# Optimization experiments

Hardware: AMD Instinct MI355X
Metric: run time of the kernel (lower is better)

## Reference

```python
import jax, jax.numpy as jnp
import numpy as np

N = 50000   # nodes
E = 800000  # edges
B = 64      # graphs in batch
IN = 128    # in_features
HID = 64    # hidden_channels
H = 4       # head_count
C = 10      # out_classes
NEG = 0.2   # leaky relu negative slope
EPS = 1e-5  # batchnorm eps (eval mode, running mean 0 / var 1)


def _gat(x, edge_index, W, a_src, a_dst, b):
    """PyG GATConv (add_self_loops=False, concat=True), eval mode (no dropout)."""
    Hh, F = a_src.shape
    xW = (x @ W).reshape(-1, Hh, F)                       # [N,H,F]
    src, dst = edge_index[0], edge_index[1]
    e = (jnp.einsum('nhf,hf->nh', xW, a_src)[src]
         + jnp.einsum('nhf,hf->nh', xW, a_dst)[dst])      # [E,H]
    e = jnp.where(e > 0, e, NEG * e)                      # leaky relu
    m = jax.ops.segment_max(e, dst, num_segments=N)       # per-dst max
    m = jnp.where(jnp.isfinite(m), m, 0.0)
    p = jnp.exp(e - m[dst])
    denom = jax.ops.segment_sum(p, dst, num_segments=N)
    alpha = p / jnp.maximum(denom[dst], 1e-16)            # edge softmax over dst
    out = jax.ops.segment_sum(alpha[:, :, None] * xW[src], dst, num_segments=N)
    return out.reshape(-1, Hh * F) + b


def _bn_relu(y, g, be):
    # BatchNorm1d in eval mode with running_mean=0, running_var=1, then ReLU
    return jax.nn.relu(g * y / jnp.sqrt(1.0 + EPS) + be)


def setup_inputs():
    key = jax.random.key(0)
    ks = jax.random.split(key, 24)
    s = lambda k, shape: (jax.random.normal(k, shape, jnp.float32) * 0.05)
    z = lambda shape: jnp.zeros(shape, jnp.float32)
    o = lambda shape: jnp.ones(shape, jnp.float32)
    return {
        'acc_flag': 0,
        'x': jax.random.normal(ks[0], (N, IN), jnp.float32),
        'edge_index': jax.random.randint(ks[1], (2, E), 0, N),
        'batch': jnp.sort(jax.random.randint(ks[2], (N,), 0, B)),
        # layer 1: GATConv(IN -> HID, heads=H, concat)
        'W1': s(ks[3], (IN, H * HID)), 'a_src1': s(ks[4], (H, HID)), 'a_dst1': s(ks[5], (H, HID)), 'b1': z((H * HID,)),
        # proj: GATConv(H*HID -> HID, heads=1) + BN
        'W2': s(ks[6], (H * HID, HID)), 'a_src2': s(ks[7], (1, HID)), 'a_dst2': s(ks[8], (1, HID)), 'b2': z((HID,)), 'g2': o((HID,)), 'be2': z((HID,)),
        # block 1
        'W3': s(ks[9], (HID, HID)), 'a_src3': s(ks[10], (1, HID)), 'a_dst3': s(ks[11], (1, HID)), 'b3': z((HID,)), 'g3': o((HID,)), 'be3': z((HID,)),
        # block 2
        'W4': s(ks[12], (HID, HID)), 'a_src4': s(ks[13], (1, HID)), 'a_dst4': s(ks[14], (1, HID)), 'b4': z((HID,)), 'g4': o((HID,)), 'be4': z((HID,)),
        # MLP head
        'Wh1': s(ks[15], (HID, 128)), 'bh1': z((128,)),
        'Wh2': s(ks[16], (128, C)), 'bh2': z((C,)),
    }


def reference(acc_flag, x, edge_index, batch,
              W1, a_src1, a_dst1, b1,
              W2, a_src2, a_dst2, b2, g2, be2,
              W3, a_src3, a_dst3, b3, g3, be3,
              W4, a_src4, a_dst4, b4, g4, be4,
              Wh1, bh1, Wh2, bh2):
    # hardware GAT layer + ReLU (relu applied twice in original -> idempotent)
    x1 = jax.nn.relu(_gat(x, edge_index, W1, a_src1, a_dst1, b1))   # [N, H*HID]
    # projection block: residual base is zeros (shape mismatch H*HID vs HID)
    h = _bn_relu(_gat(x1, edge_index, W2, a_src2, a_dst2, b2), g2, be2)
    # residual blocks (shapes match -> x + relu(bn(y)))
    h = h + _bn_relu(_gat(h, edge_index, W3, a_src3, a_dst3, b3), g3, be3)
    h = h + _bn_relu(_gat(h, edge_index, W4, a_src4, a_dst4, b4), g4, be4)
    # global mean pool over graphs
    pooled = jax.ops.segment_sum(h, batch, num_segments=B)
    cnt = jnp.maximum(jax.ops.segment_sum(jnp.ones((N,), h.dtype), batch, num_segments=B), 1.0)
    hp = pooled / cnt[:, None]                                      # [B, HID]
    # MLP head
    return jax.nn.relu(hp @ Wh1 + bh1) @ Wh2 + bh2                  # [B, C]
```

## Files before the change

### kernel.cpp

```cpp
#include <hip/hip_runtime.h>

#define N_NODES 50000
#define N_EDGES 800000
#define N_GRAPHS 64
#define F_IN 128
#define F_HID 64
#define N_HEADS 4
#define N_CLASSES 10
#define NEG_SLOPE 0.2f
#define BN_RSQ 0.9999950000374997f

typedef __bf16 bf16x8 __attribute__((ext_vector_type(8)));
typedef float floatx4 __attribute__((ext_vector_type(4)));

__device__ __forceinline__ float lrelu(float v) { return v > 0.0f ? v : NEG_SLOPE * v; }

__device__ __forceinline__ float b2f(unsigned short u) {
    return __uint_as_float(((unsigned int)u) << 16);
}
__device__ __forceinline__ unsigned short f2b(float f) {
    unsigned int u = __float_as_uint(f);
    return (unsigned short)((u + 0x7fffu + ((u >> 16) & 1u)) >> 16);
}
__device__ __forceinline__ float blo(unsigned int d) { return __uint_as_float(d << 16); }
__device__ __forceinline__ float bhi(unsigned int d) { return __uint_as_float(d & 0xffff0000u); }

__global__ void k_deg(const int* __restrict__ ei, int* __restrict__ deg) {
    int e = blockIdx.x * blockDim.x + threadIdx.x;
    if (e < N_EDGES) atomicAdd(&deg[ei[N_EDGES + e]], 1);
}

__global__ void k_offs(const int* __restrict__ deg, int* __restrict__ offs,
                       int* __restrict__ total) {
    int i = blockIdx.x * blockDim.x + threadIdx.x;
    int lane = threadIdx.x & 63;
    int v = (i < N_NODES) ? deg[i] : 0;
    int incl = v;
    for (int o = 1; o < 64; o <<= 1) {
        int t = __shfl_up(incl, o);
        if (lane >= o) incl += t;
    }
    int wtot = __shfl(incl, 63);
    int base = 0;
    if (lane == 0) base = atomicAdd(total, wtot);
    base = __shfl(base, 0);
    if (i < N_NODES) offs[i] = base + incl - v;
}

__global__ void k_fill(const int* __restrict__ ei, const int* __restrict__ offs,
                       int* __restrict__ cur, int* __restrict__ csr_src) {
    int e = blockIdx.x * blockDim.x + threadIdx.x;
    if (e < N_EDGES) {
        int d = ei[N_EDGES + e];
        int pos = offs[d] + atomicAdd(&cur[d], 1);
        csr_src[pos] = ei[e];
    }
}

__global__ void k_bounds(const int* __restrict__ batch, int* __restrict__ bounds) {
    int g = threadIdx.x;
    if (g > N_GRAPHS) return;
    int lo = 0, hi = N_NODES;
    while (lo < hi) {
        int mid = (lo + hi) >> 1;
        if (batch[mid] < g) lo = mid + 1; else hi = mid;
    }
    bounds[g] = lo;
}

__global__ void k_prepw(const float* __restrict__ W, unsigned short* __restrict__ Wt,
                        int K, int N) {
    int i = blockIdx.x * blockDim.x + threadIdx.x;
    if (i < K * N) {
        int k = i / N, n = i % N;
        Wt[n * K + k] = f2b(W[i]);
    }
}

template <int K, int N, int HEADS, bool AF32>
__global__ __launch_bounds__(256) void k_mgemm(const void* __restrict__ Ap,
                                               const unsigned short* __restrict__ Bt,
                                               const float* __restrict__ asrc,
                                               const float* __restrict__ adst,
                                               unsigned short* __restrict__ out,
                                               float* __restrict__ es,
                                               float* __restrict__ ed, int rows) {
    constexpr int LDP = K + 8;
    __shared__ unsigned short As[64 * LDP];
    const int tid = threadIdx.x;
    const int r0 = blockIdx.x * 64;
    if (AF32) {
        const float* A = (const float*)Ap;
        for (int i = tid; i < 16 * K; i += 256) {
            int r = i / (K / 4), c4 = i % (K / 4);
            int row = r0 + r;
            float4 v = (row < rows) ? *(const float4*)&A[(size_t)row * K + c4 * 4]
                                    : make_float4(0.f, 0.f, 0.f, 0.f);
            ushort4 u;
            u.x = f2b(v.x); u.y = f2b(v.y); u.z = f2b(v.z); u.w = f2b(v.w);
            *(ushort4*)&As[r * LDP + c4 * 4] = u;
        }
    } else {
        const unsigned short* A = (const unsigned short*)Ap;
        for (int i = tid; i < 8 * K; i += 256) {
            int r = i / (K / 8), c8 = i % (K / 8);
            int row = r0 + r;
            uint4 v;
            if (row < rows) v = *(const uint4*)&A[(size_t)row * K + c8 * 8];
            else { v.x = v.y = v.z = v.w = 0; }
            *(uint4*)&As[r * LDP + c8 * 8] = v;
        }
    }
    __syncthreads();
    const int w = tid >> 6, lane = tid & 63;
    const int quad = lane >> 4, l16 = lane & 15;
    const int gr0 = r0 + w * 16 + quad * 4;
    bf16x8 afrag[K / 32];
#pragma unroll
    for (int kk = 0; kk < K / 32; ++kk)
        afrag[kk] = *(const bf16x8*)&As[(w * 16 + l16) * LDP + kk * 32 + quad * 8];
    float sacc[4] = {0.f, 0.f, 0.f, 0.f};
    float dacc[4] = {0.f, 0.f, 0.f, 0.f};
#pragma unroll 1
    for (int ct = 0; ct < N / 16; ++ct) {
        floatx4 acc = {0.f, 0.f, 0.f, 0.f};
#pragma unroll
        for (int kk = 0; kk < K / 32; ++kk) {
            const bf16x8 bfrag =
                *(const bf16x8*)&Bt[(size_t)(ct * 16 + l16) * K + kk * 32 + quad * 8];
            acc = __builtin_amdgcn_mfma_f32_16x16x32_bf16(afrag[kk], bfrag, acc, 0, 0, 0);
        }
        const int gc = ct * 16 + l16;
        const int hh = gc >> 6;
        const float av = asrc[gc & (64 * HEADS > N ? N - 1 : 63) + (hh << 6) - (hh << 6)
                              ];
        (void)av;
        {
            const int f = gc & 63;
            const float as = asrc[hh * 64 + f];
            const float ad = adst[hh * 64 + f];
#pragma unroll
            for (int rg = 0; rg < 4; ++rg) {
                sacc[rg] = fmaf(acc[rg], as, sacc[rg]);
                dacc[rg] = fmaf(acc[rg], ad, dacc[rg]);
            }
        }
#pragma unroll
        for (int rg = 0; rg < 4; ++rg) {
            int gr = gr0 + rg;
            if (gr < rows) out[(size_t)gr * N + gc] = f2b(acc[rg]);
        }
        if ((ct & 3) == 3) {
#pragma unroll
            for (int rg = 0; rg < 4; ++rg) {
                float s = sacc[rg], d = dacc[rg];
                for (int o = 1; o < 16; o <<= 1) {
                    s += __shfl_xor(s, o);
                    d += __shfl_xor(d, o);
                }
                if (l16 == 0) {
                    int gr = gr0 + rg;
                    if (gr < rows) {
                        es[(size_t)gr * HEADS + hh] = s;
                        ed[(size_t)gr * HEADS + hh] = d;
                    }
                }
                sacc[rg] = 0.f;
                dacc[rg] = 0.f;
            }
        }
    }
}

__global__ __launch_bounds__(256) void k_gat1(
    const unsigned short* __restrict__ xW, const float* __restrict__ es, const float* __restrict__ ed,
    const int* __restrict__ offs, const int* __restrict__ deg, const int* __restrict__ csr,
    const float* __restrict__ bias, unsigned short* __restrict__ out) {
    __shared__ float ps[4][256];
    __shared__ int sbuf[4][64];
    const int wv = threadIdx.x >> 6;
    const int lane = threadIdx.x & 63;
    const int n = blockIdx.x * 4 + wv;
    if (n >= N_NODES) return;
    const int off = offs[n];
    const int dg = deg[n];
    const float4 edv = *(const float4*)&ed[n * 4];
    const int t = lane & 15, grp = lane >> 4, hq = t >> 2;

    float acc[16];
#pragma unroll
    for (int k = 0; k < 16; ++k) acc[k] = 0.f;
    float d0 = 0.f, d1 = 0.f, d2 = 0.f, d3 = 0.f;

    for (int base = 0; base < dg; base += 64) {
        const int idx = base + lane;
        int s_l = 0;
        float p0 = 0.f, p1 = 0.f, p2 = 0.f, p3 = 0.f;
        if (idx < dg) {
            s_l = csr[off + idx];
            const float4 ev = *(const float4*)&es[s_l * 4];
            p0 = __expf(lrelu(ev.x + edv.x));
            p1 = __expf(lrelu(ev.y + edv.y));
            p2 = __expf(lrelu(ev.z + edv.z));
            p3 = __expf(lrelu(ev.w + edv.w));
        }
        d0 += p0; d1 += p1; d2 += p2; d3 += p3;
        *(float4*)&ps[wv][lane * 4] = make_float4(p0, p1, p2, p3);
        sbuf[wv][lane] = s_l;
        const int cnt = min(64, dg - base);
        const int cntR = (cnt + 7) & ~7;
        for (int j4 = 0; j4 < cntR; j4 += 8) {
            const int ja = j4 + grp;
            const int jb = ja + 4;
            const float pa = ps[wv][ja * 4 + hq];
            const float pb = ps[wv][jb * 4 + hq];
            const int sa = sbuf[wv][ja];
            const int sb = sbuf[wv][jb];
            const uint4 a0 = *(const uint4*)&xW[(size_t)sa * 256 + t * 16];
            const uint4 a1 = *(const uint4*)&xW[(size_t)sa * 256 + t * 16 + 8];
            const uint4 b0 = *(const uint4*)&xW[(size_t)sb * 256 + t * 16];
            const uint4 b1 = *(const uint4*)&xW[(size_t)sb * 256 + t * 16 + 8];
            acc[0]  = fmaf(pa, blo(a0.x), acc[0]);
            acc[1]  = fmaf(pa, bhi(a0.x), acc[1]);
            acc[2]  = fmaf(pa, blo(a0.y), acc[2]);
            acc[3]  = fmaf(pa, bhi(a0.y), acc[3]);
            acc[4]  = fmaf(pa, blo(a0.z), acc[4]);
            acc[5]  = fmaf(pa, bhi(a0.z), acc[5]);
            acc[6]  = fmaf(pa, blo(a0.w), acc[6]);
            acc[7]  = fmaf(pa, bhi(a0.w), acc[7]);
            acc[8]  = fmaf(pa, blo(a1.x), acc[8]);
            acc[9]  = fmaf(pa, bhi(a1.x), acc[9]);
            acc[10] = fmaf(pa, blo(a1.y), acc[10]);
            acc[11] = fmaf(pa, bhi(a1.y), acc[11]);
            acc[12] = fmaf(pa, blo(a1.z), acc[12]);
            acc[13] = fmaf(pa, bhi(a1.z), acc[13]);
            acc[14] = fmaf(pa, blo(a1.w), acc[14]);
            acc[15] = fmaf(pa, bhi(a1.w), acc[15]);
            acc[0]  = fmaf(pb, blo(b0.x), acc[0]);
            acc[1]  = fmaf(pb, bhi(b0.x), acc[1]);
            acc[2]  = fmaf(pb, blo(b0.y), acc[2]);
            acc[3]  = fmaf(pb, bhi(b0.y), acc[3]);
            acc[4]  = fmaf(pb, blo(b0.z), acc[4]);
            acc[5]  = fmaf(pb, bhi(b0.z), acc[5]);
            acc[6]  = fmaf(pb, blo(b0.w), acc[6]);
            acc[7]  = fmaf(pb, bhi(b0.w), acc[7]);
            acc[8]  = fmaf(pb, blo(b1.x), acc[8]);
            acc[9]  = fmaf(pb, bhi(b1.x), acc[9]);
            acc[10] = fmaf(pb, blo(b1.y), acc[10]);
            acc[11] = fmaf(pb, bhi(b1.y), acc[11]);
            acc[12] = fmaf(pb, blo(b1.z), acc[12]);
            acc[13] = fmaf(pb, bhi(b1.z), acc[13]);
            acc[14] = fmaf(pb, blo(b1.w), acc[14]);
            acc[15] = fmaf(pb, bhi(b1.w), acc[15]);
        }
    }
#pragma unroll
    for (int k = 0; k < 16; ++k) {
        acc[k] += __shfl_xor(acc[k], 16);
        acc[k] += __shfl_xor(acc[k], 32);
    }
    for (int o = 1; o < 64; o <<= 1) {
        d0 += __shfl_xor(d0, o);
        d1 += __shfl_xor(d1, o);
        d2 += __shfl_xor(d2, o);
        d3 += __shfl_xor(d3, o);
    }
    if (grp == 0) {
        const float dsel = hq == 0 ? d0 : hq == 1 ? d1 : hq == 2 ? d2 : d3;
        const float inv = 1.0f / fmaxf(dsel, 1e-16f);
#pragma unroll
        for (int k4 = 0; k4 < 16; k4 += 4) {
            const int c = t * 16 + k4;
            const float4 bv = *(const float4*)&bias[c];
            ushort4 o4;
            o4.x = f2b(fmaxf(fmaf(acc[k4 + 0], inv, bv.x), 0.f));
            o4.y = f2b(fmaxf(fmaf(acc[k4 + 1], inv, bv.y), 0.f));
            o4.z = f2b(fmaxf(fmaf(acc[k4 + 2], inv, bv.z), 0.f));
            o4.w = f2b(fmaxf(fmaf(acc[k4 + 3], inv, bv.w), 0.f));
            *(ushort4*)&out[(size_t)n * 256 + c] = o4;
        }
    }
}

template <bool RES>
__global__ __launch_bounds__(256) void k_gatL(
    const unsigned short* __restrict__ xW, const float* __restrict__ es, const float* __restrict__ ed,
    const int* __restrict__ offs, const int* __restrict__ deg, const int* __restrict__ csr,
    const float* __restrict__ bias, const float* __restrict__ gam, const float* __restrict__ bet,
    float* __restrict__ h, unsigned short* __restrict__ hb) {
    __shared__ float ps[4][64];
    __shared__ int sbuf[4][64];
    const int wv = threadIdx.x >> 6;
    const int lane = threadIdx.x & 63;
    const int n = blockIdx.x * 4 + wv;
    if (n >= N_NODES) return;
    const int off = offs[n];
    const int dg = deg[n];
    const float edn = ed[n];
    const int t = lane & 7, grp = lane >> 3;

    float acc[8];
#pragma unroll
    for (int k = 0; k < 8; ++k) acc[k] = 0.f;
    float dsum = 0.f;

    for (int base = 0; base < dg; base += 64) {
        const int idx = base + lane;
        int s_l = 0;
        float p_l = 0.f;
        if (idx < dg) {
            s_l = csr[off + idx];
            p_l = __expf(lrelu(es[s_l] + edn));
        }
        dsum += p_l;
        ps[wv][lane] = p_l;
        sbuf[wv][lane] = s_l;
        const int cnt = min(64, dg - base);
        const int cntR = (cnt + 15) & ~15;
        for (int j8 = 0; j8 < cntR; j8 += 16) {
            const int ja = j8 + grp;
            const int jb = ja + 8;
            const float pa = ps[wv][ja];
            const float pb = ps[wv][jb];
            const int sa = sbuf[wv][ja];
            const int sb = sbuf[wv][jb];
            const uint4 a = *(const uint4*)&xW[(size_t)sa * 64 + t * 8];
            const uint4 b = *(const uint4*)&xW[(size_t)sb * 64 + t * 8];
            acc[0] = fmaf(pa, blo(a.x), acc[0]);
            acc[1] = fmaf(pa, bhi(a.x), acc[1]);
            acc[2] = fmaf(pa, blo(a.y), acc[2]);
            acc[3] = fmaf(pa, bhi(a.y), acc[3]);
            acc[4] = fmaf(pa, blo(a.z), acc[4]);
            acc[5] = fmaf(pa, bhi(a.z), acc[5]);
            acc[6] = fmaf(pa, blo(a.w), acc[6]);
            acc[7] = fmaf(pa, bhi(a.w), acc[7]);
            acc[0] = fmaf(pb, blo(b.x), acc[0]);
            acc[1] = fmaf(pb, bhi(b.x), acc[1]);
            acc[2] = fmaf(pb, blo(b.y), acc[2]);
            acc[3] = fmaf(pb, bhi(b.y), acc[3]);
            acc[4] = fmaf(pb, blo(b.z), acc[4]);
            acc[5] = fmaf(pb, bhi(b.z), acc[5]);
            acc[6] = fmaf(pb, blo(b.w), acc[6]);
            acc[7] = fmaf(pb, bhi(b.w), acc[7]);
        }
    }
#pragma unroll
    for (int k = 0; k < 8; ++k) {
        acc[k] += __shfl_xor(acc[k], 8);
        acc[k] += __shfl_xor(acc[k], 16);
        acc[k] += __shfl_xor(acc[k], 32);
    }
    for (int o = 1; o < 64; o <<= 1) dsum += __shfl_xor(dsum, o);

    if (grp == 0) {
        const float inv = 1.0f / fmaxf(dsum, 1e-16f);
        const int c0 = t * 8;
        float hn[8];
#pragma unroll
        for (int k = 0; k < 8; ++k) {
            const int c = c0 + k;
            const float y = fmaf(acc[k], inv, bias[c]);
            const float z = fmaxf(fmaf(gam[c] * y, BN_RSQ, bet[c]), 0.f);
            hn[k] = RES ? h[(size_t)n * 64 + c] + z : z;
        }
        *(float4*)&h[(size_t)n * 64 + c0] = make_float4(hn[0], hn[1], hn[2], hn[3]);
        *(float4*)&h[(size_t)n * 64 + c0 + 4] = make_float4(hn[4], hn[5], hn[6], hn[7]);
        ushort4 u0, u1;
        u0.x = f2b(hn[0]); u0.y = f2b(hn[1]); u0.z = f2b(hn[2]); u0.w = f2b(hn[3]);
        u1.x = f2b(hn[4]); u1.y = f2b(hn[5]); u1.z = f2b(hn[6]); u1.w = f2b(hn[7]);
        *(ushort4*)&hb[(size_t)n * 64 + c0] = u0;
        *(ushort4*)&hb[(size_t)n * 64 + c0 + 4] = u1;
    }
}

__global__ __launch_bounds__(256) void k_pool2(const float* __restrict__ h,
                                               const int* __restrict__ bounds,
                                               float* __restrict__ hp) {
    __shared__ float part[4][64];
    const int g = blockIdx.x;
    const int lane = threadIdx.x & 63;
    const int wid = threadIdx.x >> 6;
    const int s = bounds[g], e = bounds[g + 1];
    float acc = 0.f;
    for (int n = s + wid; n < e; n += 4) acc += h[n * 64 + lane];
    part[wid][lane] = acc;
    __syncthreads();
    if (wid == 0) {
        float v = part[0][lane] + part[1][lane] + part[2][lane] + part[3][lane];
        hp[g * 64 + lane] = v / fmaxf((float)(e - s), 1.0f);
    }
}

__global__ __launch_bounds__(256) void k_head(const float* __restrict__ hpg,
                                              const float* __restrict__ Wh1,
                                              const float* __restrict__ bh1,
                                              const float* __restrict__ Wh2,
                                              const float* __restrict__ bh2,
                                              float* __restrict__ out) {
    __shared__ float hp[64 * 64];
    __shared__ float t1[64 * 128];
    const int tid = threadIdx.x;
    for (int i = tid; i < 64 * 64; i += 256) hp[i] = hpg[i];
    __syncthreads();
    for (int i = tid; i < 64 * 128; i += 256) {
        int g = i >> 7, j = i & 127;
        float s = bh1[j];
        for (int k = 0; k < 64; ++k) s = fmaf(hp[g * 64 + k], Wh1[k * 128 + j], s);
        t1[i] = fmaxf(s, 0.f);
    }
    __syncthreads();
    for (int i = tid; i < 640; i += 256) {
        int g = i / 10, j = i - g * 10;
        float s = bh2[j];
        for (int k = 0; k < 128; ++k) s = fmaf(t1[g * 128 + k], Wh2[k * 10 + j], s);
        out[i] = s;
    }
}

extern "C" void kernel_launch(void* const* d_in, const int* in_sizes, int n_in,
                              void* d_out, int out_size, void* d_ws, size_t ws_size,
                              hipStream_t stream) {
    const float* x = (const float*)d_in[1];
    const int* ei = (const int*)d_in[2];
    const int* batch = (const int*)d_in[3];
    const float* W1 = (const float*)d_in[4];
    const float* a_src1 = (const float*)d_in[5];
    const float* a_dst1 = (const float*)d_in[6];
    const float* b1 = (const float*)d_in[7];
    const float* W2 = (const float*)d_in[8];
    const float* a_src2 = (const float*)d_in[9];
    const float* a_dst2 = (const float*)d_in[10];
    const float* b2 = (const float*)d_in[11];
    const float* g2 = (const float*)d_in[12];
    const float* be2 = (const float*)d_in[13];
    const float* W3 = (const float*)d_in[14];
    const float* a_src3 = (const float*)d_in[15];
    const float* a_dst3 = (const float*)d_in[16];
    const float* b3 = (const float*)d_in[17];
    const float* g3 = (const float*)d_in[18];
    const float* be3 = (const float*)d_in[19];
    const float* W4 = (const float*)d_in[20];
    const float* a_src4 = (const float*)d_in[21];
    const float* a_dst4 = (const float*)d_in[22];
    const float* b4 = (const float*)d_in[23];
    const float* g4 = (const float*)d_in[24];
    const float* be4 = (const float*)d_in[25];
    const float* Wh1 = (const float*)d_in[26];
    const float* bh1 = (const float*)d_in[27];
    const float* Wh2 = (const float*)d_in[28];
    const float* bh2 = (const float*)d_in[29];
    float* out = (float*)d_out;

    char* p = (char*)d_ws;
    auto alloc = [&](size_t bytes) {
        void* r = (void*)p;
        p += (bytes + 255) & ~(size_t)255;
        return r;
    };
    unsigned short* bufA = (unsigned short*)alloc((size_t)N_NODES * 256 * 2);
    unsigned short* x1b = (unsigned short*)alloc((size_t)N_NODES * 256 * 2);
    float* h = (float*)alloc((size_t)N_NODES * 64 * 4);
    unsigned short* hb = (unsigned short*)alloc((size_t)N_NODES * 64 * 2);
    float* es1 = (float*)alloc((size_t)N_NODES * 4 * 4);
    float* ed1 = (float*)alloc((size_t)N_NODES * 4 * 4);
    float* esL = (float*)alloc((size_t)N_NODES * 4);
    float* edL = (float*)alloc((size_t)N_NODES * 4);
    int* offs = (int*)alloc((size_t)N_NODES * 4);
    int* csr = (int*)alloc((size_t)N_EDGES * 4);
    int* bounds = (int*)alloc((size_t)(N_GRAPHS + 1) * 4);
    float* hpool = (float*)alloc((size_t)N_GRAPHS * 64 * 4);
    unsigned short* Wt1 = (unsigned short*)alloc((size_t)128 * 256 * 2);
    unsigned short* Wt2 = (unsigned short*)alloc((size_t)256 * 64 * 2);
    unsigned short* Wt3 = (unsigned short*)alloc((size_t)64 * 64 * 2);
    unsigned short* Wt4 = (unsigned short*)alloc((size_t)64 * 64 * 2);
    char* z0 = p;
    int* deg = (int*)alloc((size_t)N_NODES * 4);
    int* cur = (int*)alloc((size_t)N_NODES * 4);
    int* total = (int*)alloc(256);
    size_t zbytes = (size_t)(p - z0);
    hipMemsetAsync(z0, 0, zbytes, stream);

    const int edgeBlocks = (N_EDGES + 255) / 256;
    const int nodeBlocks = (N_NODES + 255) / 256;
    const int mgemmBlocks = (N_NODES + 63) / 64;
    const int gatBlocks = (N_NODES + 3) / 4;

    k_prepw<<<(128 * 256 + 255) / 256, 256, 0, stream>>>(W1, Wt1, 128, 256);
    k_prepw<<<(256 * 64 + 255) / 256, 256, 0, stream>>>(W2, Wt2, 256, 64);
    k_prepw<<<(64 * 64 + 255) / 256, 256, 0, stream>>>(W3, Wt3, 64, 64);
    k_prepw<<<(64 * 64 + 255) / 256, 256, 0, stream>>>(W4, Wt4, 64, 64);

    k_deg<<<edgeBlocks, 256, 0, stream>>>(ei, deg);
    k_offs<<<nodeBlocks, 256, 0, stream>>>(deg, offs, total);
    k_fill<<<edgeBlocks, 256, 0, stream>>>(ei, offs, cur, csr);
    k_bounds<<<1, 128, 0, stream>>>(batch, bounds);

    k_mgemm<128, 256, 4, true><<<mgemmBlocks, 256, 0, stream>>>(x, Wt1, a_src1, a_dst1,
                                                                bufA, es1, ed1, N_NODES);
    k_gat1<<<gatBlocks, 256, 0, stream>>>(bufA, es1, ed1, offs, deg, csr, b1, x1b);

    k_mgemm<256, 64, 1, false><<<mgemmBlocks, 256, 0, stream>>>(x1b, Wt2, a_src2, a_dst2,
                                                                bufA, esL, edL, N_NODES);
    k_gatL<false><<<gatBlocks, 256, 0, stream>>>(bufA, esL, edL, offs, deg, csr, b2, g2, be2, h, hb);

    k_mgemm<64, 64, 1, false><<<mgemmBlocks, 256, 0, stream>>>(hb, Wt3, a_src3, a_dst3,
                                                               bufA, esL, edL, N_NODES);
    k_gatL<true><<<gatBlocks, 256, 0, stream>>>(bufA, esL, edL, offs, deg, csr, b3, g3, be3, h, hb);

    k_mgemm<64, 64, 1, false><<<mgemmBlocks, 256, 0, stream>>>(hb, Wt4, a_src4, a_dst4,
                                                               bufA, esL, edL, N_NODES);
    k_gatL<true><<<gatBlocks, 256, 0, stream>>>(bufA, esL, edL, offs, deg, csr, b4, g4, be4, h, hb);

    k_pool2<<<N_GRAPHS, 256, 0, stream>>>(h, bounds, hpool);
    k_head<<<1, 256, 0, stream>>>(hpool, Wh1, bh1, Wh2, bh2, out);
}
```

Baseline: 543.5 us.

## Sort nodes by degree and process multiple nodes per wavefront in GAT aggregation

Builds a degree-bucketed node permutation (histogram, scan, scatter) and has each wavefront handle 4 (layer 1) or 8 (later layers) destination nodes, with 16- or 8-lane groups per node instead of a full wave per node. With an average degree of 16, a full wave mostly idled, so the change aims to improve lane utilisation and drop the cross-lane reductions. Degree sorting keeps nodes with similar degree in the same wave to limit divergence. It also merges the weight-prep launches and folds the bounds search into the offsets kernel to cut launch count, at the cost of extra preprocessing kernels and scattered output writes.

```diff
diff --git a/kernel.cpp b/kernel.cpp
--- a/kernel.cpp
+++ b/kernel.cpp
@@ -3,10 +3,6 @@
 #define N_NODES 50000
 #define N_EDGES 800000
 #define N_GRAPHS 64
-#define F_IN 128
-#define F_HID 64
-#define N_HEADS 4
-#define N_CLASSES 10
 #define NEG_SLOPE 0.2f
 #define BN_RSQ 0.9999950000374997f
 
@@ -30,8 +26,21 @@
     if (e < N_EDGES) atomicAdd(&deg[ei[N_EDGES + e]], 1);
 }
 
-__global__ void k_offs(const int* __restrict__ deg, int* __restrict__ offs,
-                       int* __restrict__ total) {
+__global__ __launch_bounds__(256) void k_offs(const int* __restrict__ deg, int* __restrict__ offs,
+                                              int* __restrict__ total, const int* __restrict__ batch,
+                                              int* __restrict__ bounds, int* __restrict__ hist) {
+    __shared__ int lh[64];
+    if (threadIdx.x < 64) lh[threadIdx.x] = 0;
+    __syncthreads();
+    if (blockIdx.x == 0 && threadIdx.x <= N_GRAPHS) {
+        int g = threadIdx.x;
+        int lo = 0, hi = N_NODES;
+        while (lo < hi) {
+            int mid = (lo + hi) >> 1;
+            if (batch[mid] < g) lo = mid + 1; else hi = mid;
+        }
+        bounds[g] = lo;
+    }
     int i = blockIdx.x * blockDim.x + threadIdx.x;
     int lane = threadIdx.x & 63;
     int v = (i < N_NODES) ? deg[i] : 0;
@@ -44,7 +53,33 @@
     int base = 0;
     if (lane == 0) base = atomicAdd(total, wtot);
     base = __shfl(base, 0);
-    if (i < N_NODES) offs[i] = base + incl - v;
+    if (i < N_NODES) {
+        offs[i] = base + incl - v;
+        atomicAdd(&lh[min(v, 63)], 1);
+    }
+    __syncthreads();
+    if (threadIdx.x < 64 && lh[threadIdx.x]) atomicAdd(&hist[threadIdx.x], lh[threadIdx.x]);
+}
+
+__global__ void k_hscan(const int* __restrict__ hist, int* __restrict__ bbase) {
+    int lane = threadIdx.x & 63;
+    int v = hist[lane];
+    int incl = v;
+    for (int o = 1; o < 64; o <<= 1) {
+        int t = __shfl_up(incl, o);
+        if (lane >= o) incl += t;
+    }
+    bbase[lane] = incl - v;
+}
+
+__global__ void k_perm(const int* __restrict__ deg, const int* __restrict__ bbase,
+                       int* __restrict__ bcur, int* __restrict__ perm) {
+    int i = blockIdx.x * blockDim.x + threadIdx.x;
+    if (i < N_NODES) {
+        int b = min(deg[i], 63);
+        int pos = bbase[b] + atomicAdd(&bcur[b], 1);
+        perm[pos] = i;
+    }
 }
 
 __global__ void k_fill(const int* __restrict__ ei, const int* __restrict__ offs,
@@ -57,23 +92,26 @@
     }
 }
 
-__global__ void k_bounds(const int* __restrict__ batch, int* __restrict__ bounds) {
-    int g = threadIdx.x;
-    if (g > N_GRAPHS) return;
-    int lo = 0, hi = N_NODES;
-    while (lo < hi) {
-        int mid = (lo + hi) >> 1;
-        if (batch[mid] < g) lo = mid + 1; else hi = mid;
-    }
-    bounds[g] = lo;
-}
-
-__global__ void k_prepw(const float* __restrict__ W, unsigned short* __restrict__ Wt,
-                        int K, int N) {
+__global__ void k_prepw(const float* __restrict__ W1, const float* __restrict__ W2,
+                        const float* __restrict__ W3, const float* __restrict__ W4,
+                        unsigned short* __restrict__ Wt1, unsigned short* __restrict__ Wt2,
+                        unsigned short* __restrict__ Wt3, unsigned short* __restrict__ Wt4) {
     int i = blockIdx.x * blockDim.x + threadIdx.x;
-    if (i < K * N) {
-        int k = i / N, n = i % N;
-        Wt[n * K + k] = f2b(W[i]);
+    if (i < 32768) {
+        int k = i >> 8, n = i & 255;
+        Wt1[n * 128 + k] = f2b(W1[i]);
+    } else if (i < 49152) {
+        int j = i - 32768;
+        int k = j >> 6, n = j & 63;
+        Wt2[n * 256 + k] = f2b(W2[j]);
+    } else if (i < 53248) {
+        int j = i - 49152;
+        int k = j >> 6, n = j & 63;
+        Wt3[n * 64 + k] = f2b(W3[j]);
+    } else if (i < 57344) {
+        int j = i - 53248;
+        int k = j >> 6, n = j & 63;
+        Wt4[n * 64 + k] = f2b(W4[j]);
     }
 }
 
@@ -132,18 +170,13 @@
         }
         const int gc = ct * 16 + l16;
         const int hh = gc >> 6;
-        const float av = asrc[gc & (64 * HEADS > N ? N - 1 : 63) + (hh << 6) - (hh << 6)
-                              ];
-        (void)av;
-        {
-            const int f = gc & 63;
-            const float as = asrc[hh * 64 + f];
-            const float ad = adst[hh * 64 + f];
-#pragma unroll
-            for (int rg = 0; rg < 4; ++rg) {
-                sacc[rg] = fmaf(acc[rg], as, sacc[rg]);
-                dacc[rg] = fmaf(acc[rg], ad, dacc[rg]);
-            }
+        const int f = gc & 63;
+        const float as = asrc[hh * 64 + f];
+        const float ad = adst[hh * 64 + f];
+#pragma unroll
+        for (int rg = 0; rg < 4; ++rg) {
+            sacc[rg] = fmaf(acc[rg], as, sacc[rg]);
+            dacc[rg] = fmaf(acc[rg], ad, dacc[rg]);
         }
 #pragma unroll
         for (int rg = 0; rg < 4; ++rg) {
@@ -175,25 +208,27 @@
 __global__ __launch_bounds__(256) void k_gat1(
     const unsigned short* __restrict__ xW, const float* __restrict__ es, const float* __restrict__ ed,
     const int* __restrict__ offs, const int* __restrict__ deg, const int* __restrict__ csr,
-    const float* __restrict__ bias, unsigned short* __restrict__ out) {
-    __shared__ float ps[4][256];
+    const int* __restrict__ perm, const float* __restrict__ bias, unsigned short* __restrict__ out) {
+    __shared__ float ps[4][4 * 68];
     __shared__ int sbuf[4][64];
     const int wv = threadIdx.x >> 6;
     const int lane = threadIdx.x & 63;
-    const int n = blockIdx.x * 4 + wv;
-    if (n >= N_NODES) return;
+    const int grp = lane >> 4, t = lane & 15;
+    const int h = t >> 2;
+    const int pidx = blockIdx.x * 16 + wv * 4 + grp;
+    if (pidx >= N_NODES) return;
+    const int n = perm[pidx];
     const int off = offs[n];
     const int dg = deg[n];
     const float4 edv = *(const float4*)&ed[n * 4];
-    const int t = lane & 15, grp = lane >> 4, hq = t >> 2;
 
     float acc[16];
 #pragma unroll
     for (int k = 0; k < 16; ++k) acc[k] = 0.f;
-    float d0 = 0.f, d1 = 0.f, d2 = 0.f, d3 = 0.f;
-
-    for (int base = 0; base < dg; base += 64) {
-        const int idx = base + lane;
+    float dsum = 0.f;
+
+    for (int base = 0; base < dg; base += 16) {
+        const int idx = base + t;
         int s_l = 0;
         float p0 = 0.f, p1 = 0.f, p2 = 0.f, p3 = 0.f;
         if (idx < dg) {
@@ -204,22 +239,20 @@
             p2 = __expf(lrelu(ev.z + edv.z));
             p3 = __expf(lrelu(ev.w + edv.w));
         }
-        d0 += p0; d1 += p1; d2 += p2; d3 += p3;
-        *(float4*)&ps[wv][lane * 4] = make_float4(p0, p1, p2, p3);
-        sbuf[wv][lane] = s_l;
-        const int cnt = min(64, dg - base);
-        const int cntR = (cnt + 7) & ~7;
-        for (int j4 = 0; j4 < cntR; j4 += 8) {
-            const int ja = j4 + grp;
-            const int jb = ja + 4;
-            const float pa = ps[wv][ja * 4 + hq];
-            const float pb = ps[wv][jb * 4 + hq];
-            const int sa = sbuf[wv][ja];
-            const int sb = sbuf[wv][jb];
+        *(float4*)&ps[wv][grp * 68 + t * 4] = make_float4(p0, p1, p2, p3);
+        sbuf[wv][grp * 16 + t] = s_l;
+        const int cnt = min(16, dg - base);
+        const int cntR = (cnt + 1) & ~1;
+        for (int j = 0; j < cntR; j += 2) {
+            const float pa = ps[wv][grp * 68 + j * 4 + h];
+            const float pb = ps[wv][grp * 68 + (j + 1) * 4 + h];
+            const int sa = sbuf[wv][grp * 16 + j];
+            const int sb = sbuf[wv][grp * 16 + j + 1];
             const uint4 a0 = *(const uint4*)&xW[(size_t)sa * 256 + t * 16];
             const uint4 a1 = *(const uint4*)&xW[(size_t)sa * 256 + t * 16 + 8];
             const uint4 b0 = *(const uint4*)&xW[(size_t)sb * 256 + t * 16];
             const uint4 b1 = *(const uint4*)&xW[(size_t)sb * 256 + t * 16 + 8];
+            dsum += pa + pb;
             acc[0]  = fmaf(pa, blo(a0.x), acc[0]);
             acc[1]  = fmaf(pa, bhi(a0.x), acc[1]);
             acc[2]  = fmaf(pa, blo(a0.y), acc[2]);
@@ -254,31 +287,17 @@
             acc[15] = fmaf(pb, bhi(b1.w), acc[15]);
         }
     }
-#pragma unroll
-    for (int k = 0; k < 16; ++k) {
-        acc[k] += __shfl_xor(acc[k], 16);
-        acc[k] += __shfl_xor(acc[k], 32);
-    }
-    for (int o = 1; o < 64; o <<= 1) {
-        d0 += __shfl_xor(d0, o);
-        d1 += __shfl_xor(d1, o);
-        d2 += __shfl_xor(d2, o);
-        d3 += __shfl_xor(d3, o);
-    }
-    if (grp == 0) {
-        const float dsel = hq == 0 ? d0 : hq == 1 ? d1 : hq == 2 ? d2 : d3;
-        const float inv = 1.0f / fmaxf(dsel, 1e-16f);
-#pragma unroll
-        for (int k4 = 0; k4 < 16; k4 += 4) {
-            const int c = t * 16 + k4;
-            const float4 bv = *(const float4*)&bias[c];
-            ushort4 o4;
-            o4.x = f2b(fmaxf(fmaf(acc[k4 + 0], inv, bv.x), 0.f));
-            o4.y = f2b(fmaxf(fmaf(acc[k4 + 1], inv, bv.y), 0.f));
-            o4.z = f2b(fmaxf(fmaf(acc[k4 + 2], inv, bv.z), 0.f));
-            o4.w = f2b(fmaxf(fmaf(acc[k4 + 3], inv, bv.w), 0.f));
-            *(ushort4*)&out[(size_t)n * 256 + c] = o4;
-        }
+    const float inv = 1.0f / fmaxf(dsum, 1e-16f);
+#pragma unroll
+    for (int k4 = 0; k4 < 16; k4 += 4) {
+        const int c = t * 16 + k4;
+        const float4 bv = *(const float4*)&bias[c];
+        ushort4 o4;
+        o4.x = f2b(fmaxf(fmaf(acc[k4 + 0], inv, bv.x), 0.f));
+        o4.y = f2b(fmaxf(fmaf(acc[k4 + 1], inv, bv.y), 0.f));
+        o4.z = f2b(fmaxf(fmaf(acc[k4 + 2], inv, bv.z), 0.f));
+        o4.w = f2b(fmaxf(fmaf(acc[k4 + 3], inv, bv.w), 0.f));
+        *(ushort4*)&out[(size_t)n * 256 + c] = o4;
     }
 }
 
@@ -286,46 +305,45 @@
 __global__ __launch_bounds__(256) void k_gatL(
     const unsigned short* __restrict__ xW, const float* __restrict__ es, const float* __restrict__ ed,
     const int* __restrict__ offs, const int* __restrict__ deg, const int* __restrict__ csr,
-    const float* __restrict__ bias, const float* __restrict__ gam, const float* __restrict__ bet,
-    float* __restrict__ h, unsigned short* __restrict__ hb) {
+    const int* __restrict__ perm, const float* __restrict__ bias, const float* __restrict__ gam,
+    const float* __restrict__ bet, float* __restrict__ h, unsigned short* __restrict__ hb) {
     __shared__ float ps[4][64];
     __shared__ int sbuf[4][64];
     const int wv = threadIdx.x >> 6;
     const int lane = threadIdx.x & 63;
-    const int n = blockIdx.x * 4 + wv;
-    if (n >= N_NODES) return;
+    const int grp = lane >> 3, t = lane & 7;
+    const int pidx = blockIdx.x * 32 + wv * 8 + grp;
+    if (pidx >= N_NODES) return;
+    const int n = perm[pidx];
     const int off = offs[n];
     const int dg = deg[n];
     const float edn = ed[n];
-    const int t = lane & 7, grp = lane >> 3;
 
     float acc[8];
 #pragma unroll
     for (int k = 0; k < 8; ++k) acc[k] = 0.f;
     float dsum = 0.f;
 
-    for (int base = 0; base < dg; base += 64) {
-        const int idx = base + lane;
+    for (int base = 0; base < dg; base += 8) {
+        const int idx = base + t;
         int s_l = 0;
         float p_l = 0.f;
         if (idx < dg) {
             s_l = csr[off + idx];
             p_l = __expf(lrelu(es[s_l] + edn));
         }
-        dsum += p_l;
-        ps[wv][lane] = p_l;
-        sbuf[wv][lane] = s_l;
-        const int cnt = min(64, dg - base);
-        const int cntR = (cnt + 15) & ~15;
-        for (int j8 = 0; j8 < cntR; j8 += 16) {
-            const int ja = j8 + grp;
-            const int jb = ja + 8;
-            const float pa = ps[wv][ja];
-            const float pb = ps[wv][jb];
-            const int sa = sbuf[wv][ja];
-            const int sb = sbuf[wv][jb];
+        ps[wv][grp * 8 + t] = p_l;
+        sbuf[wv][grp * 8 + t] = s_l;
+        const int cnt = min(8, dg - base);
+        const int cntR = (cnt + 1) & ~1;
+        for (int j = 0; j < cntR; j += 2) {
+            const float pa = ps[wv][grp * 8 + j];
+            const float pb = ps[wv][grp * 8 + j + 1];
+            const int sa = sbuf[wv][grp * 8 + j];
+            const int sb = sbuf[wv][grp * 8 + j + 1];
             const uint4 a = *(const uint4*)&xW[(size_t)sa * 64 + t * 8];
             const uint4 b = *(const uint4*)&xW[(size_t)sb * 64 + t * 8];
+            dsum += pa + pb;
             acc[0] = fmaf(pa, blo(a.x), acc[0]);
             acc[1] = fmaf(pa, bhi(a.x), acc[1]);
             acc[2] = fmaf(pa, blo(a.y), acc[2]);
@@ -344,33 +362,23 @@
             acc[7] = fmaf(pb, bhi(b.w), acc[7]);
         }
     }
+    const float inv = 1.0f / fmaxf(dsum, 1e-16f);
+    const int c0 = t * 8;
+    float hn[8];
 #pragma unroll
     for (int k = 0; k < 8; ++k) {
-        acc[k] += __shfl_xor(acc[k], 8);
-        acc[k] += __shfl_xor(acc[k], 16);
-        acc[k] += __shfl_xor(acc[k], 32);
-    }
-    for (int o = 1; o < 64; o <<= 1) dsum += __shfl_xor(dsum, o);
-
-    if (grp == 0) {
-        const float inv = 1.0f / fmaxf(dsum, 1e-16f);
-        const int c0 = t * 8;
-        float hn[8];
-#pragma unroll
-        for (int k = 0; k < 8; ++k) {
-            const int c = c0 + k;
-            const float y = fmaf(acc[k], inv, bias[c]);
-            const float z = fmaxf(fmaf(gam[c] * y, BN_RSQ, bet[c]), 0.f);
-            hn[k] = RES ? h[(size_t)n * 64 + c] + z : z;
-        }
-        *(float4*)&h[(size_t)n * 64 + c0] = make_float4(hn[0], hn[1], hn[2], hn[3]);
-        *(float4*)&h[(size_t)n * 64 + c0 + 4] = make_float4(hn[4], hn[5], hn[6], hn[7]);
-        ushort4 u0, u1;
-        u0.x = f2b(hn[0]); u0.y = f2b(hn[1]); u0.z = f2b(hn[2]); u0.w = f2b(hn[3]);
-        u1.x = f2b(hn[4]); u1.y = f2b(hn[5]); u1.z = f2b(hn[6]); u1.w = f2b(hn[7]);
-        *(ushort4*)&hb[(size_t)n * 64 + c0] = u0;
-        *(ushort4*)&hb[(size_t)n * 64 + c0 + 4] = u1;
-    }
+        const int c = c0 + k;
+        const float y = fmaf(acc[k], inv, bias[c]);
+        const float z = fmaxf(fmaf(gam[c] * y, BN_RSQ, bet[c]), 0.f);
+        hn[k] = RES ? h[(size_t)n * 64 + c] + z : z;
+    }
+    *(float4*)&h[(size_t)n * 64 + c0] = make_float4(hn[0], hn[1], hn[2], hn[3]);
+    *(float4*)&h[(size_t)n * 64 + c0 + 4] = make_float4(hn[4], hn[5], hn[6], hn[7]);
+    ushort4 u0, u1;
+    u0.x = f2b(hn[0]); u0.y = f2b(hn[1]); u0.z = f2b(hn[2]); u0.w = f2b(hn[3]);
+    u1.x = f2b(hn[4]); u1.y = f2b(hn[5]); u1.z = f2b(hn[6]); u1.w = f2b(hn[7]);
+    *(ushort4*)&hb[(size_t)n * 64 + c0] = u0;
+    *(ushort4*)&hb[(size_t)n * 64 + c0 + 4] = u1;
 }
 
 __global__ __launch_bounds__(256) void k_pool2(const float* __restrict__ h,
@@ -467,7 +475,9 @@
     float* edL = (float*)alloc((size_t)N_NODES * 4);
     int* offs = (int*)alloc((size_t)N_NODES * 4);
     int* csr = (int*)alloc((size_t)N_EDGES * 4);
+    int* perm = (int*)alloc((size_t)N_NODES * 4);
     int* bounds = (int*)alloc((size_t)(N_GRAPHS + 1) * 4);
+    int* bbase = (int*)alloc((size_t)64 * 4);
     float* hpool = (float*)alloc((size_t)N_GRAPHS * 64 * 4);
     unsigned short* Wt1 = (unsigned short*)alloc((size_t)128 * 256 * 2);
     unsigned short* Wt2 = (unsigned short*)alloc((size_t)256 * 64 * 2);
@@ -476,6 +486,8 @@
     char* z0 = p;
     int* deg = (int*)alloc((size_t)N_NODES * 4);
     int* cur = (int*)alloc((size_t)N_NODES * 4);
+    int* hist = (int*)alloc((size_t)64 * 4);
+    int* bcur = (int*)alloc((size_t)64 * 4);
     int* total = (int*)alloc(256);
     size_t zbytes = (size_t)(p - z0);
     hipMemsetAsync(z0, 0, zbytes, stream);
@@ -483,33 +495,32 @@
     const int edgeBlocks = (N_EDGES + 255) / 256;
     const int nodeBlocks = (N_NODES + 255) / 256;
     const int mgemmBlocks = (N_NODES + 63) / 64;
-    const int gatBlocks = (N_NODES + 3) / 4;
-
-    k_prepw<<<(128 * 256 + 255) / 256, 256, 0, stream>>>(W1, Wt1, 128, 256);
-    k_prepw<<<(256 * 64 + 255) / 256, 256, 0, stream>>>(W2, Wt2, 256, 64);
-    k_prepw<<<(64 * 64 + 255) / 256, 256, 0, stream>>>(W3, Wt3, 64, 64);
-    k_prepw<<<(64 * 64 + 255) / 256, 256, 0, stream>>>(W4, Wt4, 64, 64);
+    const int gat1Blocks = (N_NODES + 15) / 16;
+    const int gatLBlocks = (N_NODES + 31) / 32;
+
+    k_prepw<<<(57344 + 255) / 256, 256, 0, stream>>>(W1, W2, W3, W4, Wt1, Wt2, Wt3, Wt4);
 
     k_deg<<<edgeBlocks, 256, 0, stream>>>(ei, deg);
-    k_offs<<<nodeBlocks, 256, 0, stream>>>(deg, offs, total);
+    k_offs<<<nodeBlocks, 256, 0, stream>>>(deg, offs, total, batch, bounds, hist);
+    k_hscan<<<1, 64, 0, stream>>>(hist, bbase);
+    k_perm<<<nodeBlocks, 256, 0, stream>>>(deg, bbase, bcur, perm);
     k_fill<<<edgeBlocks, 256, 0, stream>>>(ei, offs, cur, csr);
-    k_bounds<<<1, 128, 0, stream>>>(batch, bounds);
 
     k_mgemm<128, 256, 4, true><<<mgemmBlocks, 256, 0, stream>>>(x, Wt1, a_src1, a_dst1,
                                                                 bufA, es1, ed1, N_NODES);
-    k_gat1<<<gatBlocks, 256, 0, stream>>>(bufA, es1, ed1, offs, deg, csr, b1, x1b);
+    k_gat1<<<gat1Blocks, 256, 0, stream>>>(bufA, es1, ed1, offs, deg, csr, perm, b1, x1b);
 
     k_mgemm<256, 64, 1, false><<<mgemmBlocks, 256, 0, stream>>>(x1b, Wt2, a_src2, a_dst2,
                                                                 bufA, esL, edL, N_NODES);
-    k_gatL<false><<<gatBlocks, 256, 0, stream>>>(bufA, esL, edL, offs, deg, csr, b2, g2, be2, h, hb);
+    k_gatL<false><<<gatLBlocks, 256, 0, stream>>>(bufA, esL, edL, offs, deg, csr, perm, b2, g2, be2, h, hb);
 
     k_mgemm<64, 64, 1, false><<<mgemmBlocks, 256, 0, stream>>>(hb, Wt3, a_src3, a_dst3,
                                                                bufA, esL, edL, N_NODES);
-    k_gatL<true><<<gatBlocks, 256, 0, stream>>>(bufA, esL, edL, offs, deg, csr, b3, g3, be3, h, hb);
+    k_gatL<true><<<gatLBlocks, 256, 0, stream>>>(bufA, esL, edL, offs, deg, csr, perm, b3, g3, be3, h, hb);
 
     k_mgemm<64, 64, 1, false><<<mgemmBlocks, 256, 0, stream>>>(hb, Wt4, a_src4, a_dst4,
                                                                bufA, esL, edL, N_NODES);
-    k_gatL<true><<<gatBlocks, 256, 0, stream>>>(bufA, esL, edL, offs, deg, csr, b4, g4, be4, h, hb);
+    k_gatL<true><<<gatLBlocks, 256, 0, stream>>>(bufA, esL, edL, offs, deg, csr, perm, b4, g4, be4, h, hb);
 
     k_pool2<<<N_GRAPHS, 256, 0, stream>>>(h, bounds, hpool);
     k_head<<<1, 256, 0, stream>>>(hpool, Wh1, bh1, Wh2, bh2, out);
```

Result: slower. 650.7 us (+19.7%).
